# Kernel optimization log

Measured on AMD Instinct MI355X. Metric: run time of the kernel, lower is better.

The kernel has to match this reference:

```python
import jax, jax.numpy as jnp
import numpy as np

N = 4096
NFEAT = 512
NHID = 60
NCLASS = 4


def setup_inputs() -> dict:
    key = jax.random.key(0)
    ks = jax.random.split(key, 12)
    x = jax.random.normal(ks[0], (N, NFEAT), dtype=jnp.float32)
    # sparse-ish binary adjacency (sub_adj), symmetric not required by the module
    sub_adj = (jax.random.uniform(ks[1], (N, N)) < 0.002).astype(jnp.float32)
    # P_vec: init to ones (torch.sub in reset_parameters is non-inplace, so it stays ones)
    P_vec = jnp.ones((N * (N + 1) // 2,), dtype=jnp.float32)
    s1 = 1.0 / np.sqrt(NFEAT)
    s2 = 1.0 / np.sqrt(NHID)
    W1 = jax.random.normal(ks[2], (NFEAT, NHID), dtype=jnp.float32) * s1
    b1 = jax.random.normal(ks[3], (NHID,), dtype=jnp.float32) * 0.01
    W2 = jax.random.normal(ks[4], (NHID, NHID), dtype=jnp.float32) * s2
    b2 = jax.random.normal(ks[5], (NHID,), dtype=jnp.float32) * 0.01
    W3 = jax.random.normal(ks[6], (NHID, NHID), dtype=jnp.float32) * s2
    b3 = jax.random.normal(ks[7], (NHID,), dtype=jnp.float32) * 0.01
    lin_w = jax.random.normal(ks[8], (NHID, NCLASS), dtype=jnp.float32) * s2
    lin_b = jax.random.normal(ks[9], (NCLASS,), dtype=jnp.float32) * 0.01
    return {"x": x, "sub_adj": sub_adj, "P_vec": P_vec,
            "W1": W1, "b1": b1, "W2": W2, "b2": b2, "W3": W3, "b3": b3,
            "lin_w": lin_w, "lin_b": lin_b}


def reference(x, sub_adj, P_vec, W1, b1, W2, b2, W3, b3, lin_w, lin_b):
    n = sub_adj.shape[0]
    # scatter P_vec into lower triangle (incl. diagonal), then symmetrize
    il, jl = jnp.tril_indices(n)
    M = jnp.zeros((n, n), dtype=P_vec.dtype).at[il, jl].set(P_vec)
    P_hat_symm = M + M.T - jnp.diag(jnp.diag(M))
    # perturbed adjacency with self-loops
    A_tilde = jax.nn.sigmoid(P_hat_symm) * sub_adj + jnp.eye(n, dtype=P_vec.dtype)
    # degree (column sums, matching python sum(adj)); detached in the original
    d = jax.lax.stop_gradient(jnp.sum(A_tilde, axis=0))
    d_inv_sqrt = jnp.where(d > 0, d ** -0.5, 0.0)  # isinf -> 0
    # D^{-1/2} A D^{-1/2} without materializing diag matrices
    norm_adj = d_inv_sqrt[:, None] * A_tilde * d_inv_sqrt[None, :]
    # 3 GCN layers: spmm(norm_adj, x @ W) + b
    h1 = jax.nn.relu(norm_adj @ (x @ W1) + b1)
    h2 = jax.nn.relu(norm_adj @ (h1 @ W2) + b2)
    h3 = norm_adj @ (h2 @ W3) + b3
    logits = h3 @ lin_w + lin_b  # dropout is identity in eval / p=0
    return jax.nn.log_softmax(logits, axis=1)
```

## Files before the change

### kernel.cpp

```cpp
#include <hip/hip_runtime.h>
#include <math.h>

#define NN 4096
#define NFEAT 512
#define NHID 60
#define NCLASS 4
#define CAP 96
#define GSTRIDE 64

__global__ void k_init(float* __restrict__ d, int* __restrict__ cnt) {
    int i = blockIdx.x * blockDim.x + threadIdx.x;
    if (i < NN) { d[i] = 1.0f; cnt[i] = 0; }
}

__global__ void k_scan(const float* __restrict__ adj, const float* __restrict__ P,
                       float* __restrict__ dcol, int* __restrict__ cnt,
                       int* __restrict__ cols, float* __restrict__ vals) {
    const int t  = blockIdx.x * blockDim.x + threadIdx.x;
    const int nT = gridDim.x * blockDim.x;
    #pragma unroll
    for (int u = 0; u < 4; ++u) {
        int v = u * nT + t;
        float4 a = ((const float4*)adj)[v];
        int e0 = v * 4;
        float av[4] = {a.x, a.y, a.z, a.w};
        #pragma unroll
        for (int q = 0; q < 4; ++q) {
            float aval = av[q];
            if (aval != 0.0f) {
                int e = e0 + q;
                int i = e >> 12;
                int j = e & (NN - 1);
                int hi = i >= j ? i : j;
                int lo = i >= j ? j : i;
                int pidx = ((hi * (hi + 1)) >> 1) + lo;
                float p = P[pidx];
                float s = aval / (1.0f + __expf(-p));
                atomicAdd(&dcol[j], s);
                int pos = atomicAdd(&cnt[i], 1);
                if (pos < CAP) { cols[i * CAP + pos] = j; vals[i * CAP + pos] = s; }
            }
        }
    }
}

__global__ void k_dis(const float* __restrict__ d, float* __restrict__ dis) {
    int i = blockIdx.x * blockDim.x + threadIdx.x;
    if (i < NN) {
        float v = d[i];
        dis[i] = v > 0.0f ? rsqrtf(v) : 0.0f;
    }
}

__global__ __launch_bounds__(64) void k_xw(const float* __restrict__ x,
                                           const float* __restrict__ W1,
                                           float* __restrict__ g1) {
    __shared__ float xst[NFEAT * 4];
    const int row0 = blockIdx.x * 4;
    const int tid = threadIdx.x;
    for (int f = tid; f < 4 * NFEAT; f += 64) {
        int r = f >> 9;
        int k = f & (NFEAT - 1);
        xst[k * 4 + r] = x[(row0 + r) * NFEAT + k];
    }
    __syncthreads();
    const int c = tid < NHID ? tid : NHID - 1;
    float a0 = 0.f, a1 = 0.f, a2 = 0.f, a3 = 0.f;
    for (int k = 0; k < NFEAT; ++k) {
        float w = W1[k * NHID + c];
        float4 xv = *(const float4*)&xst[k * 4];
        a0 = fmaf(xv.x, w, a0);
        a1 = fmaf(xv.y, w, a1);
        a2 = fmaf(xv.z, w, a2);
        a3 = fmaf(xv.w, w, a3);
    }
    if (tid < NHID) {
        g1[(row0 + 0) * GSTRIDE + tid] = a0;
        g1[(row0 + 1) * GSTRIDE + tid] = a1;
        g1[(row0 + 2) * GSTRIDE + tid] = a2;
        g1[(row0 + 3) * GSTRIDE + tid] = a3;
    } else {
        g1[(row0 + 0) * GSTRIDE + tid] = 0.f;
        g1[(row0 + 1) * GSTRIDE + tid] = 0.f;
        g1[(row0 + 2) * GSTRIDE + tid] = 0.f;
        g1[(row0 + 3) * GSTRIDE + tid] = 0.f;
    }
}

__global__ __launch_bounds__(64) void k_layer(const float* __restrict__ gin,
                                              float* __restrict__ gout,
                                              const float* __restrict__ dis,
                                              const int* __restrict__ cnt,
                                              const int* __restrict__ cols,
                                              const float* __restrict__ vals,
                                              const float* __restrict__ bias,
                                              const float* __restrict__ W,
                                              int relu) {
    __shared__ float hs[64];
    const int i = blockIdx.x;
    const int tid = threadIdx.x;
    const float di = dis[i];
    const int nn = min(cnt[i], CAP);
    float acc = gin[i * GSTRIDE + tid] * di;
    for (int e = 0; e < nn; ++e) {
        int j   = cols[i * CAP + e];
        float f = vals[i * CAP + e] * dis[j];
        acc = fmaf(f, gin[j * GSTRIDE + tid], acc);
    }
    acc *= di;
    if (tid < NHID) {
        acc += bias[tid];
        if (relu) acc = fmaxf(acc, 0.0f);
        hs[tid] = acc;
    } else {
        hs[tid] = 0.0f;
    }
    __syncthreads();
    float o = 0.0f;
    const int c = tid < NHID ? tid : 0;
    for (int k = 0; k < NHID; ++k)
        o = fmaf(hs[k], W[k * NHID + c], o);
    gout[i * GSTRIDE + tid] = (tid < NHID) ? o : 0.0f;
}

__global__ __launch_bounds__(64) void k_final(const float* __restrict__ gin,
                                              float* __restrict__ out,
                                              const float* __restrict__ dis,
                                              const int* __restrict__ cnt,
                                              const int* __restrict__ cols,
                                              const float* __restrict__ vals,
                                              const float* __restrict__ b3,
                                              const float* __restrict__ lw,
                                              const float* __restrict__ lb) {
    __shared__ float hs[64];
    __shared__ float lg[NCLASS];
    const int i = blockIdx.x;
    const int tid = threadIdx.x;
    const float di = dis[i];
    const int nn = min(cnt[i], CAP);
    float acc = gin[i * GSTRIDE + tid] * di;
    for (int e = 0; e < nn; ++e) {
        int j   = cols[i * CAP + e];
        float f = vals[i * CAP + e] * dis[j];
        acc = fmaf(f, gin[j * GSTRIDE + tid], acc);
    }
    acc *= di;
    hs[tid] = (tid < NHID) ? acc + b3[tid] : 0.0f;
    __syncthreads();
    if (tid < NCLASS) {
        float o = lb[tid];
        for (int k = 0; k < NHID; ++k)
            o = fmaf(hs[k], lw[k * NCLASS + tid], o);
        lg[tid] = o;
    }
    __syncthreads();
    if (tid < NCLASS) {
        float m = fmaxf(fmaxf(lg[0], lg[1]), fmaxf(lg[2], lg[3]));
        float s = expf(lg[0] - m) + expf(lg[1] - m) + expf(lg[2] - m) + expf(lg[3] - m);
        out[i * NCLASS + tid] = lg[tid] - m - logf(s);
    }
}

extern "C" void kernel_launch(void* const* d_in, const int* in_sizes, int n_in,
                              void* d_out, int out_size, void* d_ws, size_t ws_size,
                              hipStream_t stream) {
    const float* x     = (const float*)d_in[0];
    const float* adj   = (const float*)d_in[1];
    const float* P     = (const float*)d_in[2];
    const float* W1    = (const float*)d_in[3];
    const float* b1    = (const float*)d_in[4];
    const float* W2    = (const float*)d_in[5];
    const float* b2    = (const float*)d_in[6];
    const float* W3    = (const float*)d_in[7];
    const float* b3    = (const float*)d_in[8];
    const float* lw    = (const float*)d_in[9];
    const float* lb    = (const float*)d_in[10];
    float* out = (float*)d_out;

    char* ws = (char*)d_ws;
    float* d    = (float*)(ws);
    float* dis  = (float*)(ws + 16384);
    int*   cnt  = (int*)  (ws + 32768);
    int*   cols = (int*)  (ws + 49152);
    float* vals = (float*)(ws + 49152 + 1572864);
    float* bufA = (float*)(ws + 49152 + 2 * 1572864);
    float* bufB = (float*)(ws + 49152 + 2 * 1572864 + 1048576);

    k_init<<<16, 256, 0, stream>>>(d, cnt);
    k_scan<<<4096, 256, 0, stream>>>(adj, P, d, cnt, cols, vals);
    k_dis<<<16, 256, 0, stream>>>(d, dis);
    k_xw<<<1024, 64, 0, stream>>>(x, W1, bufA);
    k_layer<<<NN, 64, 0, stream>>>(bufA, bufB, dis, cnt, cols, vals, b1, W2, 1);
    k_layer<<<NN, 64, 0, stream>>>(bufB, bufA, dis, cnt, cols, vals, b2, W3, 1);
    k_final<<<NN, 64, 0, stream>>>(bufA, out, dis, cnt, cols, vals, b3, lw, lb);
}
```

Before: 201.1 us.

## Fuse all GCN stages into one cooperative persistent kernel with grid syncs

Replaces the seven separate launches (init, scan, dis, xw, two layers, final) with one cooperative persistent kernel that separates phases with grid.sync, plus a memset to zero the degree and count arrays. Odd and even blocks run the adjacency scan and the x@W1 product in opposite order so the bandwidth-bound scan overlaps the compute-bound GEMM. The scan skips all-zero float4s early, the dis kernel is removed by computing rsqrt(1+dcol) inline, and the 4-class softmax uses warp shuffles. It trades launch overhead and inter-kernel gaps for grid-wide barrier cost and limited occupancy, and also recomputes rsqrt for every neighbor lookup.

```diff
diff --git a/kernel.cpp b/kernel.cpp
--- a/kernel.cpp
+++ b/kernel.cpp
@@ -1,5 +1,8 @@
 #include <hip/hip_runtime.h>
+#include <hip/hip_cooperative_groups.h>
 #include <math.h>
+
+namespace cg = cooperative_groups;
 
 #define NN 4096
 #define NFEAT 512
@@ -8,189 +11,190 @@
 #define CAP 96
 #define GSTRIDE 64
 
-__global__ void k_init(float* __restrict__ d, int* __restrict__ cnt) {
-    int i = blockIdx.x * blockDim.x + threadIdx.x;
-    if (i < NN) { d[i] = 1.0f; cnt[i] = 0; }
-}
-
-__global__ void k_scan(const float* __restrict__ adj, const float* __restrict__ P,
-                       float* __restrict__ dcol, int* __restrict__ cnt,
-                       int* __restrict__ cols, float* __restrict__ vals) {
-    const int t  = blockIdx.x * blockDim.x + threadIdx.x;
-    const int nT = gridDim.x * blockDim.x;
-    #pragma unroll
-    for (int u = 0; u < 4; ++u) {
-        int v = u * nT + t;
-        float4 a = ((const float4*)adj)[v];
-        int e0 = v * 4;
-        float av[4] = {a.x, a.y, a.z, a.w};
+struct Params {
+    const float *x, *adj, *P, *W1, *b1, *W2, *b2, *W3, *b3, *lw, *lb;
+    float *out;
+    float *dcol; int *cnt; int *cols; float *vals; float *bufA; float *bufB;
+};
+
+__device__ __forceinline__ void scan_phase(const Params& p, int gtid, int nthreads) {
+    const int nvec = (NN * NN) / 4;
+    for (int v = gtid; v < nvec; v += nthreads) {
+        const float4 a = ((const float4*)p.adj)[v];
+        if (a.x == 0.f && a.y == 0.f && a.z == 0.f && a.w == 0.f) continue;
+        const int e0 = v * 4;
+        const float av[4] = {a.x, a.y, a.z, a.w};
         #pragma unroll
         for (int q = 0; q < 4; ++q) {
-            float aval = av[q];
-            if (aval != 0.0f) {
-                int e = e0 + q;
-                int i = e >> 12;
-                int j = e & (NN - 1);
-                int hi = i >= j ? i : j;
-                int lo = i >= j ? j : i;
-                int pidx = ((hi * (hi + 1)) >> 1) + lo;
-                float p = P[pidx];
-                float s = aval / (1.0f + __expf(-p));
-                atomicAdd(&dcol[j], s);
-                int pos = atomicAdd(&cnt[i], 1);
-                if (pos < CAP) { cols[i * CAP + pos] = j; vals[i * CAP + pos] = s; }
+            if (av[q] != 0.f) {
+                const int e = e0 + q;
+                const int i = e >> 12;
+                const int j = e & (NN - 1);
+                const int hi = i > j ? i : j;
+                const int lo = i > j ? j : i;
+                const float pv = p.P[((hi * (hi + 1)) >> 1) + lo];
+                const float s = av[q] / (1.f + __expf(-pv));
+                atomicAdd(&p.dcol[j], s);
+                const int pos = atomicAdd(&p.cnt[i], 1);
+                if (pos < CAP) { p.cols[i * CAP + pos] = j; p.vals[i * CAP + pos] = s; }
             }
         }
     }
 }
 
-__global__ void k_dis(const float* __restrict__ d, float* __restrict__ dis) {
-    int i = blockIdx.x * blockDim.x + threadIdx.x;
-    if (i < NN) {
-        float v = d[i];
-        dis[i] = v > 0.0f ? rsqrtf(v) : 0.0f;
-    }
-}
-
-__global__ __launch_bounds__(64) void k_xw(const float* __restrict__ x,
-                                           const float* __restrict__ W1,
-                                           float* __restrict__ g1) {
-    __shared__ float xst[NFEAT * 4];
-    const int row0 = blockIdx.x * 4;
+__device__ __forceinline__ void xw_phase(const Params& p, float* xst, float* part,
+                                         int w, int lane, int tid) {
+    for (int bi = blockIdx.x; bi < NN / 4; bi += gridDim.x) {
+        const int row0 = bi * 4;
+        for (int f = tid; f < 4 * NFEAT; f += 256) {
+            const int r = f >> 9, k = f & (NFEAT - 1);
+            xst[k * 4 + r] = p.x[(row0 + r) * NFEAT + k];
+        }
+        __syncthreads();
+        const int c = lane < NHID ? lane : 0;
+        float a0 = 0.f, a1 = 0.f, a2 = 0.f, a3 = 0.f;
+        const int k0 = w * (NFEAT / 4);
+        for (int k = k0; k < k0 + NFEAT / 4; ++k) {
+            const float wv = p.W1[k * NHID + c];
+            const float4 xv = *(const float4*)&xst[k * 4];
+            a0 = fmaf(xv.x, wv, a0); a1 = fmaf(xv.y, wv, a1);
+            a2 = fmaf(xv.z, wv, a2); a3 = fmaf(xv.w, wv, a3);
+        }
+        part[(w * 4 + 0) * 64 + lane] = a0;
+        part[(w * 4 + 1) * 64 + lane] = a1;
+        part[(w * 4 + 2) * 64 + lane] = a2;
+        part[(w * 4 + 3) * 64 + lane] = a3;
+        __syncthreads();
+        const float o = part[(0 * 4 + w) * 64 + lane] + part[(1 * 4 + w) * 64 + lane]
+                      + part[(2 * 4 + w) * 64 + lane] + part[(3 * 4 + w) * 64 + lane];
+        p.bufA[(row0 + w) * GSTRIDE + lane] = (lane < NHID) ? o : 0.f;
+        __syncthreads();
+    }
+}
+
+__device__ __forceinline__ void layer_phase(const Params& p, const float* gin, float* gout,
+                                            const float* bias, const float* W, bool relu,
+                                            float* hs, int w, int lane) {
+    for (int bi = blockIdx.x; bi < NN / 4; bi += gridDim.x) {
+        const int i = bi * 4 + w;
+        const float di = rsqrtf(1.f + p.dcol[i]);
+        const int nn = min(p.cnt[i], CAP);
+        float acc = gin[i * GSTRIDE + lane] * di;
+        for (int e = 0; e < nn; ++e) {
+            const int j = p.cols[i * CAP + e];
+            const float f = p.vals[i * CAP + e] * rsqrtf(1.f + p.dcol[j]);
+            acc = fmaf(f, gin[j * GSTRIDE + lane], acc);
+        }
+        acc *= di;
+        if (lane < NHID) {
+            acc += bias[lane];
+            if (relu) acc = fmaxf(acc, 0.f);
+        } else acc = 0.f;
+        hs[w * 64 + lane] = acc;
+        __syncthreads();
+        const int c = lane < NHID ? lane : 0;
+        float o = 0.f;
+        for (int k = 0; k < NHID; ++k)
+            o = fmaf(hs[w * 64 + k], W[k * NHID + c], o);
+        gout[i * GSTRIDE + lane] = (lane < NHID) ? o : 0.f;
+        __syncthreads();
+    }
+}
+
+__device__ __forceinline__ void final_phase(const Params& p, const float* gin,
+                                            float* hs, int w, int lane) {
+    for (int bi = blockIdx.x; bi < NN / 4; bi += gridDim.x) {
+        const int i = bi * 4 + w;
+        const float di = rsqrtf(1.f + p.dcol[i]);
+        const int nn = min(p.cnt[i], CAP);
+        float acc = gin[i * GSTRIDE + lane] * di;
+        for (int e = 0; e < nn; ++e) {
+            const int j = p.cols[i * CAP + e];
+            const float f = p.vals[i * CAP + e] * rsqrtf(1.f + p.dcol[j]);
+            acc = fmaf(f, gin[j * GSTRIDE + lane], acc);
+        }
+        acc *= di;
+        hs[w * 64 + lane] = (lane < NHID) ? acc + p.b3[lane] : 0.f;
+        __syncthreads();
+        if (lane < NCLASS) {
+            float o = p.lb[lane];
+            for (int k = 0; k < NHID; ++k)
+                o = fmaf(hs[w * 64 + k], p.lw[k * NCLASS + lane], o);
+            float m = fmaxf(o, __shfl_xor(o, 1));
+            m = fmaxf(m, __shfl_xor(m, 2));
+            const float ex = __expf(o - m);
+            float ssum = ex + __shfl_xor(ex, 1);
+            ssum += __shfl_xor(ssum, 2);
+            p.out[i * NCLASS + lane] = o - m - __logf(ssum);
+        }
+        __syncthreads();
+    }
+}
+
+__global__ __launch_bounds__(256, 4) void k_fused(Params p) {
+    __shared__ float smem[2048 + 1024];
+    cg::grid_group grid = cg::this_grid();
     const int tid = threadIdx.x;
-    for (int f = tid; f < 4 * NFEAT; f += 64) {
-        int r = f >> 9;
-        int k = f & (NFEAT - 1);
-        xst[k * 4 + r] = x[(row0 + r) * NFEAT + k];
-    }
-    __syncthreads();
-    const int c = tid < NHID ? tid : NHID - 1;
-    float a0 = 0.f, a1 = 0.f, a2 = 0.f, a3 = 0.f;
-    for (int k = 0; k < NFEAT; ++k) {
-        float w = W1[k * NHID + c];
-        float4 xv = *(const float4*)&xst[k * 4];
-        a0 = fmaf(xv.x, w, a0);
-        a1 = fmaf(xv.y, w, a1);
-        a2 = fmaf(xv.z, w, a2);
-        a3 = fmaf(xv.w, w, a3);
-    }
-    if (tid < NHID) {
-        g1[(row0 + 0) * GSTRIDE + tid] = a0;
-        g1[(row0 + 1) * GSTRIDE + tid] = a1;
-        g1[(row0 + 2) * GSTRIDE + tid] = a2;
-        g1[(row0 + 3) * GSTRIDE + tid] = a3;
+    const int w = tid >> 6, lane = tid & 63;
+    const int gtid = blockIdx.x * 256 + tid;
+    const int nthreads = gridDim.x * 256;
+
+    if (blockIdx.x & 1) {
+        scan_phase(p, gtid, nthreads);
+        xw_phase(p, smem, smem + 2048, w, lane, tid);
     } else {
-        g1[(row0 + 0) * GSTRIDE + tid] = 0.f;
-        g1[(row0 + 1) * GSTRIDE + tid] = 0.f;
-        g1[(row0 + 2) * GSTRIDE + tid] = 0.f;
-        g1[(row0 + 3) * GSTRIDE + tid] = 0.f;
-    }
-}
-
-__global__ __launch_bounds__(64) void k_layer(const float* __restrict__ gin,
-                                              float* __restrict__ gout,
-                                              const float* __restrict__ dis,
-                                              const int* __restrict__ cnt,
-                                              const int* __restrict__ cols,
-                                              const float* __restrict__ vals,
-                                              const float* __restrict__ bias,
-                                              const float* __restrict__ W,
-                                              int relu) {
-    __shared__ float hs[64];
-    const int i = blockIdx.x;
-    const int tid = threadIdx.x;
-    const float di = dis[i];
-    const int nn = min(cnt[i], CAP);
-    float acc = gin[i * GSTRIDE + tid] * di;
-    for (int e = 0; e < nn; ++e) {
-        int j   = cols[i * CAP + e];
-        float f = vals[i * CAP + e] * dis[j];
-        acc = fmaf(f, gin[j * GSTRIDE + tid], acc);
-    }
-    acc *= di;
-    if (tid < NHID) {
-        acc += bias[tid];
-        if (relu) acc = fmaxf(acc, 0.0f);
-        hs[tid] = acc;
-    } else {
-        hs[tid] = 0.0f;
-    }
-    __syncthreads();
-    float o = 0.0f;
-    const int c = tid < NHID ? tid : 0;
-    for (int k = 0; k < NHID; ++k)
-        o = fmaf(hs[k], W[k * NHID + c], o);
-    gout[i * GSTRIDE + tid] = (tid < NHID) ? o : 0.0f;
-}
-
-__global__ __launch_bounds__(64) void k_final(const float* __restrict__ gin,
-                                              float* __restrict__ out,
-                                              const float* __restrict__ dis,
-                                              const int* __restrict__ cnt,
-                                              const int* __restrict__ cols,
-                                              const float* __restrict__ vals,
-                                              const float* __restrict__ b3,
-                                              const float* __restrict__ lw,
-                                              const float* __restrict__ lb) {
-    __shared__ float hs[64];
-    __shared__ float lg[NCLASS];
-    const int i = blockIdx.x;
-    const int tid = threadIdx.x;
-    const float di = dis[i];
-    const int nn = min(cnt[i], CAP);
-    float acc = gin[i * GSTRIDE + tid] * di;
-    for (int e = 0; e < nn; ++e) {
-        int j   = cols[i * CAP + e];
-        float f = vals[i * CAP + e] * dis[j];
-        acc = fmaf(f, gin[j * GSTRIDE + tid], acc);
-    }
-    acc *= di;
-    hs[tid] = (tid < NHID) ? acc + b3[tid] : 0.0f;
-    __syncthreads();
-    if (tid < NCLASS) {
-        float o = lb[tid];
-        for (int k = 0; k < NHID; ++k)
-            o = fmaf(hs[k], lw[k * NCLASS + tid], o);
-        lg[tid] = o;
-    }
-    __syncthreads();
-    if (tid < NCLASS) {
-        float m = fmaxf(fmaxf(lg[0], lg[1]), fmaxf(lg[2], lg[3]));
-        float s = expf(lg[0] - m) + expf(lg[1] - m) + expf(lg[2] - m) + expf(lg[3] - m);
-        out[i * NCLASS + tid] = lg[tid] - m - logf(s);
-    }
+        xw_phase(p, smem, smem + 2048, w, lane, tid);
+        scan_phase(p, gtid, nthreads);
+    }
+    __threadfence();
+    grid.sync();
+
+    layer_phase(p, p.bufA, p.bufB, p.b1, p.W2, true, smem, w, lane);
+    __threadfence();
+    grid.sync();
+
+    layer_phase(p, p.bufB, p.bufA, p.b2, p.W3, true, smem, w, lane);
+    __threadfence();
+    grid.sync();
+
+    final_phase(p, p.bufA, smem, w, lane);
 }
 
 extern "C" void kernel_launch(void* const* d_in, const int* in_sizes, int n_in,
                               void* d_out, int out_size, void* d_ws, size_t ws_size,
                               hipStream_t stream) {
-    const float* x     = (const float*)d_in[0];
-    const float* adj   = (const float*)d_in[1];
-    const float* P     = (const float*)d_in[2];
-    const float* W1    = (const float*)d_in[3];
-    const float* b1    = (const float*)d_in[4];
-    const float* W2    = (const float*)d_in[5];
-    const float* b2    = (const float*)d_in[6];
-    const float* W3    = (const float*)d_in[7];
-    const float* b3    = (const float*)d_in[8];
-    const float* lw    = (const float*)d_in[9];
-    const float* lb    = (const float*)d_in[10];
-    float* out = (float*)d_out;
+    Params prm;
+    prm.x  = (const float*)d_in[0];
+    prm.adj = (const float*)d_in[1];
+    prm.P  = (const float*)d_in[2];
+    prm.W1 = (const float*)d_in[3];
+    prm.b1 = (const float*)d_in[4];
+    prm.W2 = (const float*)d_in[5];
+    prm.b2 = (const float*)d_in[6];
+    prm.W3 = (const float*)d_in[7];
+    prm.b3 = (const float*)d_in[8];
+    prm.lw = (const float*)d_in[9];
+    prm.lb = (const float*)d_in[10];
+    prm.out = (float*)d_out;
 
     char* ws = (char*)d_ws;
-    float* d    = (float*)(ws);
-    float* dis  = (float*)(ws + 16384);
-    int*   cnt  = (int*)  (ws + 32768);
-    int*   cols = (int*)  (ws + 49152);
-    float* vals = (float*)(ws + 49152 + 1572864);
-    float* bufA = (float*)(ws + 49152 + 2 * 1572864);
-    float* bufB = (float*)(ws + 49152 + 2 * 1572864 + 1048576);
-
-    k_init<<<16, 256, 0, stream>>>(d, cnt);
-    k_scan<<<4096, 256, 0, stream>>>(adj, P, d, cnt, cols, vals);
-    k_dis<<<16, 256, 0, stream>>>(d, dis);
-    k_xw<<<1024, 64, 0, stream>>>(x, W1, bufA);
-    k_layer<<<NN, 64, 0, stream>>>(bufA, bufB, dis, cnt, cols, vals, b1, W2, 1);
-    k_layer<<<NN, 64, 0, stream>>>(bufB, bufA, dis, cnt, cols, vals, b2, W3, 1);
-    k_final<<<NN, 64, 0, stream>>>(bufA, out, dis, cnt, cols, vals, b3, lw, lb);
-}
+    prm.dcol = (float*)ws;
+    prm.cnt  = (int*)(ws + 16384);
+    prm.cols = (int*)(ws + 32768);
+    prm.vals = (float*)(ws + 32768 + 1572864);
+    prm.bufA = (float*)(ws + 32768 + 2 * 1572864);
+    prm.bufB = (float*)(ws + 32768 + 2 * 1572864 + 1048576);
+
+    hipMemsetAsync(ws, 0, 32768, stream);
+
+    int dev = 0, numCU = 256, q = 0, maxPerCU = 4;
+    hipGetDevice(&dev);
+    hipDeviceGetAttribute(&numCU, hipDeviceAttributeMultiprocessorCount, dev);
+    if (hipOccupancyMaxActiveBlocksPerMultiprocessor(&q, k_fused, 256, 0) == hipSuccess && q > 0)
+        maxPerCU = q;
+    int nblk = numCU * maxPerCU;
+    if (nblk > NN / 4) nblk = NN / 4;
+
+    void* kp[] = { (void*)&prm };
+    hipLaunchCooperativeKernel((void*)k_fused, dim3(nblk), dim3(256), kp, 0, stream);
+}
```

New measurement: 575.3 us. 2.86x slower.
